# Optimization experiments

Hardware: AMD Instinct MI355X
Metric: run time of the kernel (lower is better)

Reference implementation:

```python
import jax, jax.numpy as jnp
import numpy as np

N = 128       # n_channels
B = 131072    # batch
C = np.float32(np.sqrt(0.5))  # 50/50 beamsplitter amplitude (c = s = sqrt(0.5))


def setup_inputs() -> dict:
    key = jax.random.key(0)
    k1, k2, k3, k4 = jax.random.split(key, 4)
    M = N * (N - 1) // 2
    return {
        "x_real": jax.random.normal(k1, (B, N), jnp.float32),
        "x_imag": jax.random.normal(k2, (B, N), jnp.float32),
        "mzi_phases": jax.random.normal(k3, (M * 2,), jnp.float32) * 0.1,
        "output_phases": jax.random.normal(k4, (N,), jnp.float32) * 0.1,
    }


def _construct_unitary(mzi_phases, output_phases):
    n = output_phases.shape[0]
    m = n * (n - 1) // 2
    # pair ordering matches the torch double loop: i ascending, then j > i (row-major triu)
    i_np, j_np = np.triu_indices(n, 1)
    i_idx = jnp.asarray(i_np, jnp.int32)
    j_idx = jnp.asarray(j_np, jnp.int32)
    ph = mzi_phases.reshape(m, 2)
    theta, phi = ph[:, 0], ph[:, 1]

    def step(U, xs):
        th, ph_, i, j = xs
        e_phi = jax.lax.complex(jnp.cos(ph_), jnp.sin(ph_))
        e_th = jax.lax.complex(jnp.cos(th), jnp.sin(th))
        ri = U[i]
        rj = U[j]
        # T_ij @ U touches only rows i and j (O(N) Givens row update)
        new_i = C * ri + (C * e_phi) * rj
        new_j = (C * e_th) * ri - (C * e_th * e_phi) * rj
        U = U.at[i].set(new_i).at[j].set(new_j)
        return U, None

    def chunk_body(U, xs_chunk):
        U, _ = jax.lax.scan(step, U, xs_chunk)
        return U, None

    # chunk the M sequential updates: M = (n-1) * (n//2) for even n;
    # checkpointing chunks keeps reverse-mode memory O(sqrt-ish) instead of O(M * N^2)
    n_chunks = n - 1
    cs = n // 2
    xs = (theta.reshape(n_chunks, cs), phi.reshape(n_chunks, cs),
          i_idx.reshape(n_chunks, cs), j_idx.reshape(n_chunks, cs))
    U0 = jnp.eye(n, dtype=jnp.complex64)
    U, _ = jax.lax.scan(jax.checkpoint(chunk_body), U0, xs)
    # output phase screen D @ U
    d = jax.lax.complex(jnp.cos(output_phases), jnp.sin(output_phases))
    return d[:, None] * U


def reference(x_real, x_imag, mzi_phases, output_phases):
    U = _construct_unitary(mzi_phases, output_phases)           # [N, N] complex64
    x = jax.lax.complex(x_real, x_imag)                          # [B, N] complex64
    # matmul(U, x.unsqueeze(-1)).squeeze(-1) == x @ U^T
    out = jnp.einsum('nm,bm->bn', U, x)                          # [B, N] complex64
    # ComplexDropout is identity in eval mode
    return out
```

## Files before the change

### kernel.cpp

```cpp
#include <hip/hip_runtime.h>
#include <hip/hip_bf16.h>

#define NDIM 128
#define BDIM 131072
#define NMZI 8128
#define NCHUNK 8
#define NJG 8
#define NCOL 32
#define NLOC 16
static constexpr float CC = 0.70710678118654752440f;

typedef __attribute__((ext_vector_type(8))) short bf16x8;
typedef __attribute__((ext_vector_type(4))) float f32x4;

__device__ __align__(16) float2         g_V[NCHUNK * NDIM * NDIM];
__device__ __align__(16) float2         g_W[4 * NDIM * NDIM];
__device__ __align__(16) float2         g_Y[2 * NDIM * NDIM];
__device__ __align__(16) unsigned short g_TB[32 * NDIM * 8];
__device__ __align__(16) unsigned short g_Ur[16 * NDIM * 8];
__device__ __align__(16) unsigned short g_Ui[16 * NDIM * 8];

__device__ inline unsigned short f2bf(float f) {
    union { __hip_bfloat16 h; unsigned short u; } cv;
    cv.h = __float2bfloat16(f);
    return cv.u;
}

__global__ __launch_bounds__(256) void build_scan(const float* __restrict__ mzi) {
    __shared__ float2 Usm[NDIM][NCOL];
    __shared__ float4 ph[2][NDIM];
    __shared__ float4 comp[NJG][NCOL];
    const int tid   = threadIdx.x;
    const int c     = tid & 31;
    const int g     = tid >> 5;
    const int col0  = blockIdx.x * NCOL;
    const int chunk = blockIdx.y;
    const int i0    = chunk * 16;

    for (int k = g; k < NDIM; k += NJG)
        Usm[k][c] = make_float2((k == col0 + c) ? 1.f : 0.f, 0.f);

    const float2* mzp = (const float2*)mzi;
    int base = 127 * i0 - (i0 * (i0 - 1)) / 2;
    {
        const int L0 = NDIM - 1 - i0;
        if (tid < L0) {
            const float2 mz = mzp[base + tid];
            float sp, cp, st, ct;
            sincosf(mz.y, &sp, &cp);
            sincosf(mz.x, &st, &ct);
            ph[0][tid] = make_float4(cp, sp, CC * ct, CC * st);
        }
    }
    __syncthreads();

    #pragma unroll 1
    for (int sw = 0; sw < 16; ++sw) {
        const int i = i0 + sw;
        const int L = NDIM - 1 - i;
        if (L <= 0) break;
        const int cur = sw & 1;

        float2 mznext;
        const bool have = (sw < 15) && (tid < L - 1);
        if (have) mznext = mzp[base + L + tid];

        const float2 r0 = Usm[i][c];
        const int nloc  = (L + NJG - 1) >> 3;
        const int myBeg = g * nloc;
        const int myN   = max(0, min(nloc, L - myBeg));

        float2 treg[NLOC];
        float2 qth[NLOC];
        float  A = 1.f;
        float2 Bc = make_float2(0.f, 0.f);
        #pragma unroll
        for (int kk = 0; kk < NLOC; ++kk) {
            if (kk < myN) {
                const int off = myBeg + kk;
                const float4 q  = ph[cur][off];
                const float2 rj = Usm[i + 1 + off][c];
                const float tr = fmaf(q.x, rj.x, -q.y * rj.y);
                const float ti = fmaf(q.x, rj.y,  q.y * rj.x);
                treg[kk] = make_float2(tr, ti);
                qth[kk]  = make_float2(q.z, q.w);
                Bc.x = CC * (Bc.x + tr);
                Bc.y = CC * (Bc.y + ti);
                A *= CC;
            }
        }
        comp[g][c] = make_float4(A, Bc.x, Bc.y, 0.f);
        __syncthreads();

        float2 r = r0;
        for (int h = 0; h < g; ++h) {
            const float4 cm = comp[h][c];
            r.x = fmaf(cm.x, r.x, cm.y);
            r.y = fmaf(cm.x, r.y, cm.z);
        }

        #pragma unroll
        for (int kk = 0; kk < NLOC; ++kk) {
            if (kk < myN) {
                const float2 t = treg[kk];
                const float2 q = qth[kk];
                const float dr = r.x - t.x, di = r.y - t.y;
                const float njx = fmaf(q.x, dr, -q.y * di);
                const float njy = fmaf(q.x, di,  q.y * dr);
                Usm[i + 1 + myBeg + kk][c] = make_float2(njx, njy);
                r.x = CC * (r.x + t.x);
                r.y = CC * (r.y + t.y);
            }
        }
        if (myN > 0 && (myBeg + myN == L))
            Usm[i][c] = r;

        if (have) {
            float sp, cp, st, ct;
            sincosf(mznext.y, &sp, &cp);
            sincosf(mznext.x, &st, &ct);
            ph[cur ^ 1][tid] = make_float4(cp, sp, CC * ct, CC * st);
        }
        __syncthreads();
        base += L;
    }

    float2* Vp = g_V + chunk * NDIM * NDIM;
    for (int k = g; k < NDIM; k += NJG)
        Vp[k * NDIM + col0 + c] = Usm[k][c];
}

__global__ __launch_bounds__(128) void compose(int level) {
    const int p = blockIdx.y, n = blockIdx.x, m = threadIdx.x;
    const float2* A; const float2* B; float2* Cout;
    if (level == 0) {
        A = g_V + (2 * p + 1) * NDIM * NDIM;
        B = g_V + (2 * p) * NDIM * NDIM;
        Cout = g_W + p * NDIM * NDIM;
    } else {
        A = g_W + (2 * p + 1) * NDIM * NDIM;
        B = g_W + (2 * p) * NDIM * NDIM;
        Cout = g_Y + p * NDIM * NDIM;
    }
    __shared__ float2 arow[NDIM];
    arow[m] = A[n * NDIM + m];
    __syncthreads();
    float cr = 0.f, ci = 0.f;
    #pragma unroll 8
    for (int k = 0; k < NDIM; ++k) {
        const float2 b = B[k * NDIM + m];
        const float2 a = arow[k];
        cr = fmaf(a.x, b.x, fmaf(-a.y, b.y, cr));
        ci = fmaf(a.x, b.y, fmaf( a.y, b.x, ci));
    }
    Cout[n * NDIM + m] = make_float2(cr, ci);
}

__global__ __launch_bounds__(128) void compose_final(const float* __restrict__ oph) {
    const int n = blockIdx.x, m = threadIdx.x;
    const float2* A = g_Y + NDIM * NDIM;
    const float2* B = g_Y;
    __shared__ float2 arow[NDIM];
    arow[m] = A[n * NDIM + m];
    __syncthreads();
    float cr = 0.f, ci = 0.f;
    #pragma unroll 8
    for (int k = 0; k < NDIM; ++k) {
        const float2 b = B[k * NDIM + m];
        const float2 a = arow[k];
        cr = fmaf(a.x, b.x, fmaf(-a.y, b.y, cr));
        ci = fmaf(a.x, b.y, fmaf( a.y, b.x, ci));
    }
    float ds, dc;
    sincosf(oph[n], &ds, &dc);
    const float vr = fmaf(cr, dc, -ci * ds);
    const float vi = fmaf(cr, ds,  ci * dc);
    const int kg = m >> 3, e = m & 7;
    g_TB[(kg * NDIM + n) * 8 + e]        = f2bf(vr);
    g_TB[((16 + kg) * NDIM + n) * 8 + e] = f2bf(-vi);
    g_Ur[(kg * NDIM + n) * 8 + e] = f2bf(vr);
    g_Ui[(kg * NDIM + n) * 8 + e] = f2bf(vi);
}

__global__ __launch_bounds__(256) void cmatmul0(const float* __restrict__ xr,
                                                const float* __restrict__ xi,
                                                float* __restrict__ out) {
    __shared__ __align__(16) char smX[4][8192];
    const int tid  = threadIdx.x;
    const int lane = tid & 63;
    const int w    = tid >> 6;
    const int r15  = lane & 15;
    const int kg4  = lane >> 4;
    const int l31  = lane & 31;
    const int lh   = lane >> 5;
    const int R    = blockIdx.x * 64 + w * 16;

    const f32x4* sre = (const f32x4*)(xr + (size_t)R * NDIM);
    const f32x4* sim = (const f32x4*)(xi + (size_t)R * NDIM);
    f32x4 G[16];
    #pragma unroll
    for (int p = 0; p < 8; ++p) G[p]     = __builtin_nontemporal_load(sre + p * 64 + lane);
    #pragma unroll
    for (int p = 0; p < 8; ++p) G[8 + p] = __builtin_nontemporal_load(sim + p * 64 + lane);

    char* buf = &smX[w][0];
    #pragma unroll
    for (int p = 0; p < 8; ++p) {
        const int row = 2 * p + lh;
        const int swz = (row & 7) << 4;
        uint2 v;
        v.x = ((unsigned)f2bf(G[p][1]) << 16) | f2bf(G[p][0]);
        v.y = ((unsigned)f2bf(G[p][3]) << 16) | f2bf(G[p][2]);
        *(uint2*)(buf + row * 512 + ((l31 * 8) ^ swz)) = v;
        v.x = ((unsigned)f2bf(G[8 + p][1]) << 16) | f2bf(G[8 + p][0]);
        v.y = ((unsigned)f2bf(G[8 + p][3]) << 16) | f2bf(G[8 + p][2]);
        *(uint2*)(buf + row * 512 + 256 + ((l31 * 8) ^ swz)) = v;
    }

    bf16x8 fx[8];
    const int rswz = (r15 & 7) << 4;
    #pragma unroll
    for (int kc = 0; kc < 8; ++kc) {
        const int off = (((kc & 3) * 64 + kg4 * 16) ^ rswz) + ((kc >= 4) ? 256 : 0);
        fx[kc] = *(const bf16x8*)(buf + r15 * 512 + off);
    }

    const bf16x8* gT = (const bf16x8*)g_TB;
    #pragma unroll
    for (int nt = 0; nt < 8; ++nt) {
        f32x4 a0 = {0.f, 0.f, 0.f, 0.f};
        f32x4 a1 = {0.f, 0.f, 0.f, 0.f};
        #pragma unroll
        for (int kc = 0; kc < 4; ++kc)
            a0 = __builtin_amdgcn_mfma_f32_16x16x32_bf16(
                gT[(kc * 4 + kg4) * NDIM + nt * 16 + r15], fx[kc], a0, 0, 0, 0);
        #pragma unroll
        for (int kc = 4; kc < 8; ++kc)
            a1 = __builtin_amdgcn_mfma_f32_16x16x32_bf16(
                gT[(kc * 4 + kg4) * NDIM + nt * 16 + r15], fx[kc], a1, 0, 0, 0);
        const f32x4 s = a0 + a1;
        *(f32x4*)(buf + r15 * 512 + ((nt * 64 + kg4 * 16) ^ rswz)) = s;
    }

    char* outp = (char*)(out + (size_t)R * NDIM);
    #pragma unroll
    for (int p = 0; p < 8; ++p) {
        const int bofs = p * 1024 + lane * 16;
        const int row  = bofs >> 9;
        const int colb = bofs & 511;
        const f32x4 v = *(const f32x4*)(buf + row * 512 + (colb ^ ((row & 7) << 4)));
        __builtin_nontemporal_store(v, (f32x4*)(outp + bofs));
    }
}

__global__ __launch_bounds__(256) void cmatmul1(const float* __restrict__ xr,
                                                const float* __restrict__ xi,
                                                ushort2* __restrict__ outp) {
    const int lane  = threadIdx.x & 63;
    const int w     = threadIdx.x >> 6;
    const int btile = blockIdx.x * 64 + w * 16;
    const int r15   = lane & 15;
    const int kg4   = lane >> 4;
    const int bload = btile + r15;

    const bf16x8* Ur = (const bf16x8*)g_Ur;
    const bf16x8* Ui = (const bf16x8*)g_Ui;
    const float* xrp = xr + (size_t)bload * NDIM;
    const float* xip = xi + (size_t)bload * NDIM;

    bf16x8 ar[4], ai[4], ain[4];
    #pragma unroll
    for (int kc = 0; kc < 4; ++kc) {
        const int k0 = kc * 32 + kg4 * 8;
        float4 rlo = *(const float4*)(xrp + k0);
        float4 rhi = *(const float4*)(xrp + k0 + 4);
        float4 ilo = *(const float4*)(xip + k0);
        float4 ihi = *(const float4*)(xip + k0 + 4);
        bf16x8 vr, vi, vn;
        vr[0] = (short)f2bf(rlo.x); vr[1] = (short)f2bf(rlo.y);
        vr[2] = (short)f2bf(rlo.z); vr[3] = (short)f2bf(rlo.w);
        vr[4] = (short)f2bf(rhi.x); vr[5] = (short)f2bf(rhi.y);
        vr[6] = (short)f2bf(rhi.z); vr[7] = (short)f2bf(rhi.w);
        vi[0] = (short)f2bf(ilo.x); vi[1] = (short)f2bf(ilo.y);
        vi[2] = (short)f2bf(ilo.z); vi[3] = (short)f2bf(ilo.w);
        vi[4] = (short)f2bf(ihi.x); vi[5] = (short)f2bf(ihi.y);
        vi[6] = (short)f2bf(ihi.z); vi[7] = (short)f2bf(ihi.w);
        #pragma unroll
        for (int e = 0; e < 8; ++e) vn[e] = (short)(vi[e] ^ 0x8000);
        ar[kc] = vr; ai[kc] = vi; ain[kc] = vn;
    }

    #pragma unroll
    for (int nt = 0; nt < 8; ++nt) {
        f32x4 accR = {0.f, 0.f, 0.f, 0.f};
        f32x4 accI = {0.f, 0.f, 0.f, 0.f};
        #pragma unroll
        for (int kc = 0; kc < 4; ++kc) {
            const int kg = kc * 4 + kg4;
            bf16x8 br = Ur[kg * NDIM + nt * 16 + r15];
            bf16x8 bi = Ui[kg * NDIM + nt * 16 + r15];
            accR = __builtin_amdgcn_mfma_f32_16x16x32_bf16(ar[kc],  br, accR, 0, 0, 0);
            accR = __builtin_amdgcn_mfma_f32_16x16x32_bf16(ain[kc], bi, accR, 0, 0, 0);
            accI = __builtin_amdgcn_mfma_f32_16x16x32_bf16(ar[kc],  bi, accI, 0, 0, 0);
            accI = __builtin_amdgcn_mfma_f32_16x16x32_bf16(ai[kc],  br, accI, 0, 0, 0);
        }
        const int n    = nt * 16 + r15;
        const int brow = btile + kg4 * 4;
        #pragma unroll
        for (int r = 0; r < 4; ++r)
            outp[(size_t)(brow + r) * NDIM + n] = make_ushort2(f2bf(accR[r]), f2bf(accI[r]));
    }
}

extern "C" void kernel_launch(void* const* d_in, const int* in_sizes, int n_in,
                              void* d_out, int out_size, void* d_ws, size_t ws_size,
                              hipStream_t stream) {
    const float* xr  = (const float*)d_in[0];
    const float* xi  = (const float*)d_in[1];
    const float* mzi = (const float*)d_in[2];
    const float* oph = (const float*)d_in[3];

    build_scan<<<dim3(4, NCHUNK), dim3(256), 0, stream>>>(mzi);
    compose<<<dim3(NDIM, 4), dim3(128), 0, stream>>>(0);
    compose<<<dim3(NDIM, 2), dim3(128), 0, stream>>>(1);
    compose_final<<<dim3(NDIM), dim3(128), 0, stream>>>(oph);
    if (out_size == BDIM * NDIM) {
        cmatmul0<<<dim3(BDIM / 64), dim3(256), 0, stream>>>(xr, xi, (float*)d_out);
    } else {
        cmatmul1<<<dim3(BDIM / 64), dim3(256), 0, stream>>>(xr, xi, (ushort2*)d_out);
    }
}
```

Measured before the change: 108.8 us.

## Fuse chunk composition into one kernel and double-process tiles in cmatmul0

Replaces the three-level tree of compose launches with one kernel in which each output row does a sequential row-vector times matrix chain over the 8 chunk unitaries, with the k-sum split across two thread halves. This removes two kernel launches and the intermediate global buffers. cmatmul0 now handles two 16-row tiles per wave and issues the second tile's global loads before computing the first, so load latency overlaps with MFMA work. The cost is higher register pressure from holding the prefetched data, and half as many blocks.

```diff
diff --git a/kernel.cpp b/kernel.cpp
--- a/kernel.cpp
+++ b/kernel.cpp
@@ -14,8 +14,6 @@
 typedef __attribute__((ext_vector_type(4))) float f32x4;
 
 __device__ __align__(16) float2         g_V[NCHUNK * NDIM * NDIM];
-__device__ __align__(16) float2         g_W[4 * NDIM * NDIM];
-__device__ __align__(16) float2         g_Y[2 * NDIM * NDIM];
 __device__ __align__(16) unsigned short g_TB[32 * NDIM * 8];
 __device__ __align__(16) unsigned short g_Ur[16 * NDIM * 8];
 __device__ __align__(16) unsigned short g_Ui[16 * NDIM * 8];
@@ -130,57 +128,118 @@
         Vp[k * NDIM + col0 + c] = Usm[k][c];
 }
 
-__global__ __launch_bounds__(128) void compose(int level) {
-    const int p = blockIdx.y, n = blockIdx.x, m = threadIdx.x;
-    const float2* A; const float2* B; float2* Cout;
-    if (level == 0) {
-        A = g_V + (2 * p + 1) * NDIM * NDIM;
-        B = g_V + (2 * p) * NDIM * NDIM;
-        Cout = g_W + p * NDIM * NDIM;
-    } else {
-        A = g_W + (2 * p + 1) * NDIM * NDIM;
-        B = g_W + (2 * p) * NDIM * NDIM;
-        Cout = g_Y + p * NDIM * NDIM;
-    }
-    __shared__ float2 arow[NDIM];
-    arow[m] = A[n * NDIM + m];
+__global__ __launch_bounds__(256) void compose_all(const float* __restrict__ oph) {
+    __shared__ float2 vbuf[NDIM];
+    __shared__ float2 part[2][NDIM];
+    const int tid = threadIdx.x;
+    const int m   = tid & 127;
+    const int h   = tid >> 7;
+    const int n   = blockIdx.x;
+
+    if (h == 0) vbuf[m] = g_V[7 * NDIM * NDIM + n * NDIM + m];
     __syncthreads();
-    float cr = 0.f, ci = 0.f;
-    #pragma unroll 8
-    for (int k = 0; k < NDIM; ++k) {
-        const float2 b = B[k * NDIM + m];
-        const float2 a = arow[k];
-        cr = fmaf(a.x, b.x, fmaf(-a.y, b.y, cr));
-        ci = fmaf(a.x, b.y, fmaf( a.y, b.x, ci));
-    }
-    Cout[n * NDIM + m] = make_float2(cr, ci);
-}
-
-__global__ __launch_bounds__(128) void compose_final(const float* __restrict__ oph) {
-    const int n = blockIdx.x, m = threadIdx.x;
-    const float2* A = g_Y + NDIM * NDIM;
-    const float2* B = g_Y;
-    __shared__ float2 arow[NDIM];
-    arow[m] = A[n * NDIM + m];
-    __syncthreads();
-    float cr = 0.f, ci = 0.f;
-    #pragma unroll 8
-    for (int k = 0; k < NDIM; ++k) {
-        const float2 b = B[k * NDIM + m];
-        const float2 a = arow[k];
-        cr = fmaf(a.x, b.x, fmaf(-a.y, b.y, cr));
-        ci = fmaf(a.x, b.y, fmaf( a.y, b.x, ci));
-    }
-    float ds, dc;
-    sincosf(oph[n], &ds, &dc);
-    const float vr = fmaf(cr, dc, -ci * ds);
-    const float vi = fmaf(cr, ds,  ci * dc);
-    const int kg = m >> 3, e = m & 7;
-    g_TB[(kg * NDIM + n) * 8 + e]        = f2bf(vr);
-    g_TB[((16 + kg) * NDIM + n) * 8 + e] = f2bf(-vi);
-    g_Ur[(kg * NDIM + n) * 8 + e] = f2bf(vr);
-    g_Ui[(kg * NDIM + n) * 8 + e] = f2bf(vi);
-}
+
+    #pragma unroll 1
+    for (int c = 6; c >= 0; --c) {
+        const float2* Vc = g_V + c * NDIM * NDIM;
+        float cr = 0.f, ci = 0.f;
+        #pragma unroll 16
+        for (int k0 = 0; k0 < 64; ++k0) {
+            const int k = h * 64 + k0;
+            const float2 a = vbuf[k];
+            const float2 b = Vc[k * NDIM + m];
+            cr = fmaf(a.x, b.x, fmaf(-a.y, b.y, cr));
+            ci = fmaf(a.x, b.y, fmaf( a.y, b.x, ci));
+        }
+        part[h][m] = make_float2(cr, ci);
+        __syncthreads();
+        if (h == 0) {
+            const float2 p0 = part[0][m], p1 = part[1][m];
+            vbuf[m] = make_float2(p0.x + p1.x, p0.y + p1.y);
+        }
+        __syncthreads();
+    }
+
+    if (h == 0) {
+        const float2 u = vbuf[m];
+        float ds, dc;
+        sincosf(oph[n], &ds, &dc);
+        const float vr = fmaf(u.x, dc, -u.y * ds);
+        const float vi = fmaf(u.x, ds,  u.y * dc);
+        const int kg = m >> 3, e = m & 7;
+        g_TB[(kg * NDIM + n) * 8 + e]        = f2bf(vr);
+        g_TB[((16 + kg) * NDIM + n) * 8 + e] = f2bf(-vi);
+        g_Ur[(kg * NDIM + n) * 8 + e] = f2bf(vr);
+        g_Ui[(kg * NDIM + n) * 8 + e] = f2bf(vi);
+    }
+}
+
+#define XLOAD(G, R)                                                             \
+    {                                                                           \
+        const f32x4* sre_ = (const f32x4*)(xr + (size_t)(R) * NDIM);            \
+        const f32x4* sim_ = (const f32x4*)(xi + (size_t)(R) * NDIM);            \
+        _Pragma("unroll")                                                       \
+        for (int p_ = 0; p_ < 8; ++p_)                                          \
+            G[p_] = __builtin_nontemporal_load(sre_ + p_ * 64 + lane);          \
+        _Pragma("unroll")                                                       \
+        for (int p_ = 0; p_ < 8; ++p_)                                          \
+            G[8 + p_] = __builtin_nontemporal_load(sim_ + p_ * 64 + lane);      \
+    }
+
+#define XSTAGE(G)                                                               \
+    {                                                                           \
+        _Pragma("unroll")                                                       \
+        for (int p_ = 0; p_ < 8; ++p_) {                                        \
+            const int row_ = 2 * p_ + lh;                                       \
+            const int swz_ = (row_ & 7) << 4;                                   \
+            uint2 v_;                                                           \
+            v_.x = ((unsigned)f2bf(G[p_][1]) << 16) | f2bf(G[p_][0]);           \
+            v_.y = ((unsigned)f2bf(G[p_][3]) << 16) | f2bf(G[p_][2]);           \
+            *(uint2*)(buf + row_ * 512 + ((l31 * 8) ^ swz_)) = v_;              \
+            v_.x = ((unsigned)f2bf(G[8 + p_][1]) << 16) | f2bf(G[8 + p_][0]);   \
+            v_.y = ((unsigned)f2bf(G[8 + p_][3]) << 16) | f2bf(G[8 + p_][2]);   \
+            *(uint2*)(buf + row_ * 512 + 256 + ((l31 * 8) ^ swz_)) = v_;        \
+        }                                                                       \
+    }
+
+#define XFRAGS(fx)                                                              \
+    {                                                                           \
+        _Pragma("unroll")                                                       \
+        for (int kc_ = 0; kc_ < 8; ++kc_) {                                     \
+            const int off_ = (((kc_ & 3) * 64 + kg4 * 16) ^ rswz)               \
+                             + ((kc_ >= 4) ? 256 : 0);                          \
+            fx[kc_] = *(const bf16x8*)(buf + r15 * 512 + off_);                 \
+        }                                                                       \
+    }
+
+#define XCOMPUTE(fx, R)                                                         \
+    {                                                                           \
+        _Pragma("unroll")                                                       \
+        for (int nt_ = 0; nt_ < 8; ++nt_) {                                     \
+            f32x4 a0_ = {0.f, 0.f, 0.f, 0.f};                                   \
+            f32x4 a1_ = {0.f, 0.f, 0.f, 0.f};                                   \
+            _Pragma("unroll")                                                   \
+            for (int kc_ = 0; kc_ < 4; ++kc_)                                   \
+                a0_ = __builtin_amdgcn_mfma_f32_16x16x32_bf16(                  \
+                    gT[(kc_ * 4 + kg4) * NDIM + nt_ * 16 + r15], fx[kc_], a0_, 0, 0, 0); \
+            _Pragma("unroll")                                                   \
+            for (int kc_ = 4; kc_ < 8; ++kc_)                                   \
+                a1_ = __builtin_amdgcn_mfma_f32_16x16x32_bf16(                  \
+                    gT[(kc_ * 4 + kg4) * NDIM + nt_ * 16 + r15], fx[kc_], a1_, 0, 0, 0); \
+            const f32x4 s_ = a0_ + a1_;                                         \
+            *(f32x4*)(buf + r15 * 512 + ((nt_ * 64 + kg4 * 16) ^ rswz)) = s_;   \
+        }                                                                       \
+        char* outp_ = (char*)(out + (size_t)(R) * NDIM);                        \
+        _Pragma("unroll")                                                       \
+        for (int p_ = 0; p_ < 8; ++p_) {                                        \
+            const int bofs_ = p_ * 1024 + lane * 16;                            \
+            const int row_  = bofs_ >> 9;                                       \
+            const int colb_ = bofs_ & 511;                                      \
+            const f32x4 v_ = *(const f32x4*)(buf + row_ * 512 +                 \
+                                (colb_ ^ ((row_ & 7) << 4)));                   \
+            __builtin_nontemporal_store(v_, (f32x4*)(outp_ + bofs_));           \
+        }                                                                       \
+    }
 
 __global__ __launch_bounds__(256) void cmatmul0(const float* __restrict__ xr,
                                                 const float* __restrict__ xi,
@@ -193,64 +252,25 @@
     const int kg4  = lane >> 4;
     const int l31  = lane & 31;
     const int lh   = lane >> 5;
-    const int R    = blockIdx.x * 64 + w * 16;
-
-    const f32x4* sre = (const f32x4*)(xr + (size_t)R * NDIM);
-    const f32x4* sim = (const f32x4*)(xi + (size_t)R * NDIM);
-    f32x4 G[16];
-    #pragma unroll
-    for (int p = 0; p < 8; ++p) G[p]     = __builtin_nontemporal_load(sre + p * 64 + lane);
-    #pragma unroll
-    for (int p = 0; p < 8; ++p) G[8 + p] = __builtin_nontemporal_load(sim + p * 64 + lane);
+    const int rswz = (r15 & 7) << 4;
+    const int R0   = blockIdx.x * 128 + w * 16;
+    const int R1   = R0 + 64;
 
     char* buf = &smX[w][0];
-    #pragma unroll
-    for (int p = 0; p < 8; ++p) {
-        const int row = 2 * p + lh;
-        const int swz = (row & 7) << 4;
-        uint2 v;
-        v.x = ((unsigned)f2bf(G[p][1]) << 16) | f2bf(G[p][0]);
-        v.y = ((unsigned)f2bf(G[p][3]) << 16) | f2bf(G[p][2]);
-        *(uint2*)(buf + row * 512 + ((l31 * 8) ^ swz)) = v;
-        v.x = ((unsigned)f2bf(G[8 + p][1]) << 16) | f2bf(G[8 + p][0]);
-        v.y = ((unsigned)f2bf(G[8 + p][3]) << 16) | f2bf(G[8 + p][2]);
-        *(uint2*)(buf + row * 512 + 256 + ((l31 * 8) ^ swz)) = v;
-    }
-
+    const bf16x8* gT = (const bf16x8*)g_TB;
+
+    float4 Gt[16];
+    f32x4* G = (f32x4*)Gt;
+
+    XLOAD(G, R0)
+    XSTAGE(G)
     bf16x8 fx[8];
-    const int rswz = (r15 & 7) << 4;
-    #pragma unroll
-    for (int kc = 0; kc < 8; ++kc) {
-        const int off = (((kc & 3) * 64 + kg4 * 16) ^ rswz) + ((kc >= 4) ? 256 : 0);
-        fx[kc] = *(const bf16x8*)(buf + r15 * 512 + off);
-    }
-
-    const bf16x8* gT = (const bf16x8*)g_TB;
-    #pragma unroll
-    for (int nt = 0; nt < 8; ++nt) {
-        f32x4 a0 = {0.f, 0.f, 0.f, 0.f};
-        f32x4 a1 = {0.f, 0.f, 0.f, 0.f};
-        #pragma unroll
-        for (int kc = 0; kc < 4; ++kc)
-            a0 = __builtin_amdgcn_mfma_f32_16x16x32_bf16(
-                gT[(kc * 4 + kg4) * NDIM + nt * 16 + r15], fx[kc], a0, 0, 0, 0);
-        #pragma unroll
-        for (int kc = 4; kc < 8; ++kc)
-            a1 = __builtin_amdgcn_mfma_f32_16x16x32_bf16(
-                gT[(kc * 4 + kg4) * NDIM + nt * 16 + r15], fx[kc], a1, 0, 0, 0);
-        const f32x4 s = a0 + a1;
-        *(f32x4*)(buf + r15 * 512 + ((nt * 64 + kg4 * 16) ^ rswz)) = s;
-    }
-
-    char* outp = (char*)(out + (size_t)R * NDIM);
-    #pragma unroll
-    for (int p = 0; p < 8; ++p) {
-        const int bofs = p * 1024 + lane * 16;
-        const int row  = bofs >> 9;
-        const int colb = bofs & 511;
-        const f32x4 v = *(const f32x4*)(buf + row * 512 + (colb ^ ((row & 7) << 4)));
-        __builtin_nontemporal_store(v, (f32x4*)(outp + bofs));
-    }
+    XFRAGS(fx)
+    XLOAD(G, R1)
+    XCOMPUTE(fx, R0)
+    XSTAGE(G)
+    XFRAGS(fx)
+    XCOMPUTE(fx, R1)
 }
 
 __global__ __launch_bounds__(256) void cmatmul1(const float* __restrict__ xr,
@@ -321,11 +341,9 @@
     const float* oph = (const float*)d_in[3];
 
     build_scan<<<dim3(4, NCHUNK), dim3(256), 0, stream>>>(mzi);
-    compose<<<dim3(NDIM, 4), dim3(128), 0, stream>>>(0);
-    compose<<<dim3(NDIM, 2), dim3(128), 0, stream>>>(1);
-    compose_final<<<dim3(NDIM), dim3(128), 0, stream>>>(oph);
+    compose_all<<<dim3(NDIM), dim3(256), 0, stream>>>(oph);
     if (out_size == BDIM * NDIM) {
-        cmatmul0<<<dim3(BDIM / 64), dim3(256), 0, stream>>>(xr, xi, (float*)d_out);
+        cmatmul0<<<dim3(BDIM / 128), dim3(256), 0, stream>>>(xr, xi, (float*)d_out);
     } else {
         cmatmul1<<<dim3(BDIM / 64), dim3(256), 0, stream>>>(xr, xi, (ushort2*)d_out);
     }
```

Result: slower. 199.8 us (+83.5%).

## Fuse unitary build and compose kernels into one persistent kernel with grid barriers

Applied to the files above, without the earlier changes.

Merges build_scan, the two compose levels and compose_final into a single 32-block kernel that separates phases with atomic-counter grid barriers instead of separate launches. The compose step is restructured so each block computes four output rows per unit and prefetches B rows into registers. Barrier counters are reset by the following matmul kernel. This removes three kernel launches and their gaps, but the compose stages now run on only 32 blocks instead of 128-512, and correctness depends on all 32 blocks being co-resident and on the counters being zero on the first call.

```diff
diff --git a/kernel.cpp b/kernel.cpp
--- a/kernel.cpp
+++ b/kernel.cpp
@@ -2,9 +2,11 @@
 #include <hip/hip_bf16.h>
 
 #define NDIM 128
+#define N2   (NDIM * NDIM)
 #define BDIM 131072
 #define NMZI 8128
 #define NCHUNK 8
+#define NBLK 32
 #define NJG 8
 #define NCOL 32
 #define NLOC 16
@@ -13,12 +15,13 @@
 typedef __attribute__((ext_vector_type(8))) short bf16x8;
 typedef __attribute__((ext_vector_type(4))) float f32x4;
 
-__device__ __align__(16) float2         g_V[NCHUNK * NDIM * NDIM];
-__device__ __align__(16) float2         g_W[4 * NDIM * NDIM];
-__device__ __align__(16) float2         g_Y[2 * NDIM * NDIM];
+__device__ __align__(16) float2         g_V[NCHUNK * N2];
+__device__ __align__(16) float2         g_W[4 * N2];
+__device__ __align__(16) float2         g_Y[2 * N2];
 __device__ __align__(16) unsigned short g_TB[32 * NDIM * 8];
 __device__ __align__(16) unsigned short g_Ur[16 * NDIM * 8];
 __device__ __align__(16) unsigned short g_Ui[16 * NDIM * 8];
+__device__ unsigned g_ctr[3];
 
 __device__ inline unsigned short f2bf(float f) {
     union { __hip_bfloat16 h; unsigned short u; } cv;
@@ -26,165 +29,227 @@
     return cv.u;
 }
 
-__global__ __launch_bounds__(256) void build_scan(const float* __restrict__ mzi) {
-    __shared__ float2 Usm[NDIM][NCOL];
-    __shared__ float4 ph[2][NDIM];
-    __shared__ float4 comp[NJG][NCOL];
-    const int tid   = threadIdx.x;
-    const int c     = tid & 31;
-    const int g     = tid >> 5;
-    const int col0  = blockIdx.x * NCOL;
-    const int chunk = blockIdx.y;
-    const int i0    = chunk * 16;
-
-    for (int k = g; k < NDIM; k += NJG)
-        Usm[k][c] = make_float2((k == col0 + c) ? 1.f : 0.f, 0.f);
-
-    const float2* mzp = (const float2*)mzi;
-    int base = 127 * i0 - (i0 * (i0 - 1)) / 2;
+__device__ __forceinline__ void gbar(int idx) {
+    __syncthreads();
+    asm volatile("" ::: "memory");
+    if (threadIdx.x == 0) {
+        __threadfence();
+        __hip_atomic_fetch_add(&g_ctr[idx], 1u, __ATOMIC_ACQ_REL, __HIP_MEMORY_SCOPE_AGENT);
+        while (__hip_atomic_load(&g_ctr[idx], __ATOMIC_ACQUIRE, __HIP_MEMORY_SCOPE_AGENT)
+               < (unsigned)NBLK)
+            __builtin_amdgcn_s_sleep(8);
+        __threadfence();
+    }
+    __syncthreads();
+    asm volatile("" ::: "memory");
+}
+
+#define CFMA(acc, av, b)                                                    \
+    acc.x = fmaf(av.x, b.x, fmaf(-av.y, b.y, acc.x));                       \
+    acc.y = fmaf(av.x, b.y, fmaf( av.y, b.x, acc.y));
+
+template <int MODE>
+__device__ __forceinline__ void compose_unit(const float2* __restrict__ A,
+                                             const float2* __restrict__ B,
+                                             float2* __restrict__ Cout,
+                                             const float* __restrict__ oph,
+                                             int n0, int m, float2* __restrict__ As,
+                                             bool active) {
+    __syncthreads();
+    if (active) {
+        #pragma unroll
+        for (int r = 0; r < 4; ++r) As[r * NDIM + m] = A[(n0 + r) * NDIM + m];
+    }
+    __syncthreads();
+    if (!active) return;
+
+    float2 a0 = {0.f, 0.f}, a1 = {0.f, 0.f}, a2 = {0.f, 0.f}, a3 = {0.f, 0.f};
+    float2 bb[8];
+    #pragma unroll
+    for (int u = 0; u < 8; ++u) bb[u] = B[u * NDIM + m];
+
+    #pragma unroll 1
+    for (int k0 = 0; k0 < NDIM; k0 += 8) {
+        #pragma unroll
+        for (int u = 0; u < 8; ++u) {
+            const float2 b = bb[u];
+            bb[u] = B[(k0 + 8 + u) * NDIM + m];
+            const int k = k0 + u;
+            float2 v;
+            v = As[0 * NDIM + k]; CFMA(a0, v, b)
+            v = As[1 * NDIM + k]; CFMA(a1, v, b)
+            v = As[2 * NDIM + k]; CFMA(a2, v, b)
+            v = As[3 * NDIM + k]; CFMA(a3, v, b)
+        }
+    }
+    if (MODE == 0) {
+        Cout[(n0 + 0) * NDIM + m] = a0;
+        Cout[(n0 + 1) * NDIM + m] = a1;
+        Cout[(n0 + 2) * NDIM + m] = a2;
+        Cout[(n0 + 3) * NDIM + m] = a3;
+    } else {
+        const int kg = m >> 3, e = m & 7;
+        #pragma unroll
+        for (int r = 0; r < 4; ++r) {
+            const int n = n0 + r;
+            const float2 u = (r == 0) ? a0 : (r == 1) ? a1 : (r == 2) ? a2 : a3;
+            float ds, dc;
+            sincosf(oph[n], &ds, &dc);
+            const float vr = fmaf(u.x, dc, -u.y * ds);
+            const float vi = fmaf(u.x, ds,  u.y * dc);
+            g_TB[(kg * NDIM + n) * 8 + e]        = f2bf(vr);
+            g_TB[((16 + kg) * NDIM + n) * 8 + e] = f2bf(-vi);
+            g_Ur[(kg * NDIM + n) * 8 + e] = f2bf(vr);
+            g_Ui[(kg * NDIM + n) * 8 + e] = f2bf(vi);
+        }
+    }
+}
+
+__global__ __launch_bounds__(256) void build_all(const float* __restrict__ mzi,
+                                                 const float* __restrict__ oph) {
+    __shared__ __align__(16) char SM[40960];
+    const int tid = threadIdx.x;
+    const int b   = blockIdx.x;
+
     {
-        const int L0 = NDIM - 1 - i0;
-        if (tid < L0) {
-            const float2 mz = mzp[base + tid];
-            float sp, cp, st, ct;
-            sincosf(mz.y, &sp, &cp);
-            sincosf(mz.x, &st, &ct);
-            ph[0][tid] = make_float4(cp, sp, CC * ct, CC * st);
-        }
-    }
-    __syncthreads();
+        float2 (*Usm)[NCOL] = reinterpret_cast<float2(*)[NCOL]>(SM);
+        float4 (*ph)[NDIM]  = reinterpret_cast<float4(*)[NDIM]>(SM + 32768);
+        float4 (*cmp)[NCOL] = reinterpret_cast<float4(*)[NCOL]>(SM + 36864);
+        const int c     = tid & 31;
+        const int g     = tid >> 5;
+        const int col0  = (b & 3) * NCOL;
+        const int chunk = b >> 2;
+        const int i0    = chunk * 16;
+
+        for (int k = g; k < NDIM; k += NJG)
+            Usm[k][c] = make_float2((k == col0 + c) ? 1.f : 0.f, 0.f);
+
+        const float2* mzp = (const float2*)mzi;
+        int base = 127 * i0 - (i0 * (i0 - 1)) / 2;
+        {
+            const int L0 = NDIM - 1 - i0;
+            if (tid < L0) {
+                const float2 mz = mzp[base + tid];
+                float sp, cp, st, ct;
+                sincosf(mz.y, &sp, &cp);
+                sincosf(mz.x, &st, &ct);
+                ph[0][tid] = make_float4(cp, sp, CC * ct, CC * st);
+            }
+        }
+        __syncthreads();
+
+        #pragma unroll 1
+        for (int sw = 0; sw < 16; ++sw) {
+            const int i = i0 + sw;
+            const int L = NDIM - 1 - i;
+            if (L <= 0) break;
+            const int cur = sw & 1;
+
+            float2 mznext;
+            const bool have = (sw < 15) && (tid < L - 1);
+            if (have) mznext = mzp[base + L + tid];
+
+            const float2 r0 = Usm[i][c];
+            const int nloc  = (L + NJG - 1) >> 3;
+            const int myBeg = g * nloc;
+            const int myN   = max(0, min(nloc, L - myBeg));
+
+            float2 treg[NLOC];
+            float2 qth[NLOC];
+            float  A = 1.f;
+            float2 Bc = make_float2(0.f, 0.f);
+            #pragma unroll
+            for (int kk = 0; kk < NLOC; ++kk) {
+                if (kk < myN) {
+                    const int off = myBeg + kk;
+                    const float4 q  = ph[cur][off];
+                    const float2 rj = Usm[i + 1 + off][c];
+                    const float tr = fmaf(q.x, rj.x, -q.y * rj.y);
+                    const float ti = fmaf(q.x, rj.y,  q.y * rj.x);
+                    treg[kk] = make_float2(tr, ti);
+                    qth[kk]  = make_float2(q.z, q.w);
+                    Bc.x = CC * (Bc.x + tr);
+                    Bc.y = CC * (Bc.y + ti);
+                    A *= CC;
+                }
+            }
+            cmp[g][c] = make_float4(A, Bc.x, Bc.y, 0.f);
+            __syncthreads();
+
+            float2 r = r0;
+            for (int h2 = 0; h2 < g; ++h2) {
+                const float4 cm = cmp[h2][c];
+                r.x = fmaf(cm.x, r.x, cm.y);
+                r.y = fmaf(cm.x, r.y, cm.z);
+            }
+
+            #pragma unroll
+            for (int kk = 0; kk < NLOC; ++kk) {
+                if (kk < myN) {
+                    const float2 t = treg[kk];
+                    const float2 q = qth[kk];
+                    const float dr = r.x - t.x, di = r.y - t.y;
+                    const float njx = fmaf(q.x, dr, -q.y * di);
+                    const float njy = fmaf(q.x, di,  q.y * dr);
+                    Usm[i + 1 + myBeg + kk][c] = make_float2(njx, njy);
+                    r.x = CC * (r.x + t.x);
+                    r.y = CC * (r.y + t.y);
+                }
+            }
+            if (myN > 0 && (myBeg + myN == L))
+                Usm[i][c] = r;
+
+            if (have) {
+                float sp, cp, st, ct;
+                sincosf(mznext.y, &sp, &cp);
+                sincosf(mznext.x, &st, &ct);
+                ph[cur ^ 1][tid] = make_float4(cp, sp, CC * ct, CC * st);
+            }
+            __syncthreads();
+            base += L;
+        }
+
+        float2* Vp = g_V + chunk * N2;
+        for (int k = g; k < NDIM; k += NJG)
+            Vp[k * NDIM + col0 + c] = Usm[k][c];
+    }
+
+    gbar(0);
+
+    const int h = tid >> 7;
+    const int m = tid & 127;
+    float2* As = (float2*)(SM + h * 4096);
 
     #pragma unroll 1
-    for (int sw = 0; sw < 16; ++sw) {
-        const int i = i0 + sw;
-        const int L = NDIM - 1 - i;
-        if (L <= 0) break;
-        const int cur = sw & 1;
-
-        float2 mznext;
-        const bool have = (sw < 15) && (tid < L - 1);
-        if (have) mznext = mzp[base + L + tid];
-
-        const float2 r0 = Usm[i][c];
-        const int nloc  = (L + NJG - 1) >> 3;
-        const int myBeg = g * nloc;
-        const int myN   = max(0, min(nloc, L - myBeg));
-
-        float2 treg[NLOC];
-        float2 qth[NLOC];
-        float  A = 1.f;
-        float2 Bc = make_float2(0.f, 0.f);
-        #pragma unroll
-        for (int kk = 0; kk < NLOC; ++kk) {
-            if (kk < myN) {
-                const int off = myBeg + kk;
-                const float4 q  = ph[cur][off];
-                const float2 rj = Usm[i + 1 + off][c];
-                const float tr = fmaf(q.x, rj.x, -q.y * rj.y);
-                const float ti = fmaf(q.x, rj.y,  q.y * rj.x);
-                treg[kk] = make_float2(tr, ti);
-                qth[kk]  = make_float2(q.z, q.w);
-                Bc.x = CC * (Bc.x + tr);
-                Bc.y = CC * (Bc.y + ti);
-                A *= CC;
-            }
-        }
-        comp[g][c] = make_float4(A, Bc.x, Bc.y, 0.f);
-        __syncthreads();
-
-        float2 r = r0;
-        for (int h = 0; h < g; ++h) {
-            const float4 cm = comp[h][c];
-            r.x = fmaf(cm.x, r.x, cm.y);
-            r.y = fmaf(cm.x, r.y, cm.z);
-        }
-
-        #pragma unroll
-        for (int kk = 0; kk < NLOC; ++kk) {
-            if (kk < myN) {
-                const float2 t = treg[kk];
-                const float2 q = qth[kk];
-                const float dr = r.x - t.x, di = r.y - t.y;
-                const float njx = fmaf(q.x, dr, -q.y * di);
-                const float njy = fmaf(q.x, di,  q.y * dr);
-                Usm[i + 1 + myBeg + kk][c] = make_float2(njx, njy);
-                r.x = CC * (r.x + t.x);
-                r.y = CC * (r.y + t.y);
-            }
-        }
-        if (myN > 0 && (myBeg + myN == L))
-            Usm[i][c] = r;
-
-        if (have) {
-            float sp, cp, st, ct;
-            sincosf(mznext.y, &sp, &cp);
-            sincosf(mznext.x, &st, &ct);
-            ph[cur ^ 1][tid] = make_float4(cp, sp, CC * ct, CC * st);
-        }
-        __syncthreads();
-        base += L;
-    }
-
-    float2* Vp = g_V + chunk * NDIM * NDIM;
-    for (int k = g; k < NDIM; k += NJG)
-        Vp[k * NDIM + col0 + c] = Usm[k][c];
-}
-
-__global__ __launch_bounds__(128) void compose(int level) {
-    const int p = blockIdx.y, n = blockIdx.x, m = threadIdx.x;
-    const float2* A; const float2* B; float2* Cout;
-    if (level == 0) {
-        A = g_V + (2 * p + 1) * NDIM * NDIM;
-        B = g_V + (2 * p) * NDIM * NDIM;
-        Cout = g_W + p * NDIM * NDIM;
-    } else {
-        A = g_W + (2 * p + 1) * NDIM * NDIM;
-        B = g_W + (2 * p) * NDIM * NDIM;
-        Cout = g_Y + p * NDIM * NDIM;
-    }
-    __shared__ float2 arow[NDIM];
-    arow[m] = A[n * NDIM + m];
-    __syncthreads();
-    float cr = 0.f, ci = 0.f;
-    #pragma unroll 8
-    for (int k = 0; k < NDIM; ++k) {
-        const float2 b = B[k * NDIM + m];
-        const float2 a = arow[k];
-        cr = fmaf(a.x, b.x, fmaf(-a.y, b.y, cr));
-        ci = fmaf(a.x, b.y, fmaf( a.y, b.x, ci));
-    }
-    Cout[n * NDIM + m] = make_float2(cr, ci);
-}
-
-__global__ __launch_bounds__(128) void compose_final(const float* __restrict__ oph) {
-    const int n = blockIdx.x, m = threadIdx.x;
-    const float2* A = g_Y + NDIM * NDIM;
-    const float2* B = g_Y;
-    __shared__ float2 arow[NDIM];
-    arow[m] = A[n * NDIM + m];
-    __syncthreads();
-    float cr = 0.f, ci = 0.f;
-    #pragma unroll 8
-    for (int k = 0; k < NDIM; ++k) {
-        const float2 b = B[k * NDIM + m];
-        const float2 a = arow[k];
-        cr = fmaf(a.x, b.x, fmaf(-a.y, b.y, cr));
-        ci = fmaf(a.x, b.y, fmaf( a.y, b.x, ci));
-    }
-    float ds, dc;
-    sincosf(oph[n], &ds, &dc);
-    const float vr = fmaf(cr, dc, -ci * ds);
-    const float vi = fmaf(cr, ds,  ci * dc);
-    const int kg = m >> 3, e = m & 7;
-    g_TB[(kg * NDIM + n) * 8 + e]        = f2bf(vr);
-    g_TB[((16 + kg) * NDIM + n) * 8 + e] = f2bf(-vi);
-    g_Ur[(kg * NDIM + n) * 8 + e] = f2bf(vr);
-    g_Ui[(kg * NDIM + n) * 8 + e] = f2bf(vi);
+    for (int pass = 0; pass < 2; ++pass) {
+        const int u  = pass * 64 + 2 * b + h;
+        const int p  = u >> 5;
+        const int n0 = (u & 31) * 4;
+        compose_unit<0>(g_V + (2 * p + 1) * N2, g_V + (2 * p) * N2,
+                        g_W + p * N2, nullptr, n0, m, As, true);
+    }
+
+    gbar(1);
+
+    {
+        const int u  = 2 * b + h;
+        const int p  = u >> 5;
+        const int n0 = (u & 31) * 4;
+        compose_unit<0>(g_W + (2 * p + 1) * N2, g_W + (2 * p) * N2,
+                        g_Y + p * N2, nullptr, n0, m, As, true);
+    }
+
+    gbar(2);
+
+    compose_unit<1>(g_Y + N2, g_Y, nullptr, oph, b * 4, m, As, h == 0);
 }
 
 __global__ __launch_bounds__(256) void cmatmul0(const float* __restrict__ xr,
                                                 const float* __restrict__ xi,
                                                 float* __restrict__ out) {
+    if (blockIdx.x == 0 && threadIdx.x == 0) {
+        g_ctr[0] = 0; g_ctr[1] = 0; g_ctr[2] = 0;
+    }
     __shared__ __align__(16) char smX[4][8192];
     const int tid  = threadIdx.x;
     const int lane = tid & 63;
@@ -256,6 +321,9 @@
 __global__ __launch_bounds__(256) void cmatmul1(const float* __restrict__ xr,
                                                 const float* __restrict__ xi,
                                                 ushort2* __restrict__ outp) {
+    if (blockIdx.x == 0 && threadIdx.x == 0) {
+        g_ctr[0] = 0; g_ctr[1] = 0; g_ctr[2] = 0;
+    }
     const int lane  = threadIdx.x & 63;
     const int w     = threadIdx.x >> 6;
     const int btile = blockIdx.x * 64 + w * 16;
@@ -320,10 +388,7 @@
     const float* mzi = (const float*)d_in[2];
     const float* oph = (const float*)d_in[3];
 
-    build_scan<<<dim3(4, NCHUNK), dim3(256), 0, stream>>>(mzi);
-    compose<<<dim3(NDIM, 4), dim3(128), 0, stream>>>(0);
-    compose<<<dim3(NDIM, 2), dim3(128), 0, stream>>>(1);
-    compose_final<<<dim3(NDIM), dim3(128), 0, stream>>>(oph);
+    build_all<<<dim3(NBLK), dim3(256), 0, stream>>>(mzi, oph);
     if (out_size == BDIM * NDIM) {
         cmatmul0<<<dim3(BDIM / 64), dim3(256), 0, stream>>>(xr, xi, (float*)d_out);
     } else {
```

Measured after the change: 130.6 us. +20.0%, slower.
